# Kernel optimization log

Measured on AMD Instinct MI355X. Metric: run time of the kernel, lower is better.

## Reference

```python
import jax, jax.numpy as jnp
import numpy as np

N, H, V = 4096, 1024, 16384


def setup_inputs() -> dict:
    key = jax.random.key(0)
    k1, k2, k3, k4 = jax.random.split(key, 4)
    _input = jax.random.normal(k1, (N, H), dtype=jnp.float32)
    weight = jax.random.normal(k2, (V, H), dtype=jnp.float32) * (1.0 / np.sqrt(H))
    target = jax.random.normal(k3, (N, V), dtype=jnp.float32)
    bias = jax.random.normal(k4, (V,), dtype=jnp.float32)
    return {"_input": _input, "weight": weight, "target": target, "bias": bias}


def reference(_input, weight, target, bias):
    # Fused linear + MSE with reduction='mean':
    # logits = _input @ weight.T + bias  -> (N, V)
    # loss = mean((logits - target)**2) over all N*V elements
    logits = jnp.einsum("nh,vh->nv", _input, weight) + bias
    diff = logits - target
    return jnp.mean(diff * diff)
```

## Files before the change

### kernel.cpp

```cpp
#include <hip/hip_runtime.h>
#include <hip/hip_bf16.h>
#include <stdint.h>

#define N_ 4096
#define H_ 1024
#define V_ 16384

using bf16x8 = __attribute__((ext_vector_type(8))) short;
using f32x4  = __attribute__((ext_vector_type(4))) float;

__device__ inline ushort f2bf(float f) {
    union { float f; uint32_t u; } v; v.f = f;
    uint32_t u = v.u;
    uint32_t lsb = (u >> 16) & 1u;
    u += 0x7fffu + lsb;
    return (ushort)(u >> 16);
}

__global__ void cast_f32_to_bf16(const float* __restrict__ in, ushort* __restrict__ out) {
    size_t i = ((size_t)blockIdx.x * blockDim.x + threadIdx.x) * 8;
    float4 a = *(const float4*)(in + i);
    float4 b = *(const float4*)(in + i + 4);
    union { ushort h[8]; uint4 u; } p;
    p.h[0] = f2bf(a.x); p.h[1] = f2bf(a.y); p.h[2] = f2bf(a.z); p.h[3] = f2bf(a.w);
    p.h[4] = f2bf(b.x); p.h[5] = f2bf(b.y); p.h[6] = f2bf(b.z); p.h[7] = f2bf(b.w);
    *(uint4*)(out + i) = p.u;
}

#define BM 128
#define BN 128
#define BK 32

__global__ __launch_bounds__(256, 2) void gemm_mse(
    const ushort* __restrict__ Abf,
    const ushort* __restrict__ Wbf,
    const float*  __restrict__ target,
    const float*  __restrict__ bias,
    float* __restrict__ partials)
{
    __shared__ ushort As[BM * BK];
    __shared__ ushort Bs[BN * BK];
    __shared__ float red[4];

    const int tid  = threadIdx.x;
    const int w    = tid >> 6;
    const int lane = tid & 63;
    const int quad = lane >> 4;
    const int l16  = lane & 15;
    const int wm   = w >> 1;
    const int wn   = w & 1;

    const int rowBase = blockIdx.y * BM;
    const int colBase = blockIdx.x * BN;

    f32x4 acc[4][4];
#pragma unroll
    for (int i = 0; i < 4; ++i)
#pragma unroll
        for (int j = 0; j < 4; ++j) acc[i][j] = (f32x4){0.f, 0.f, 0.f, 0.f};

    const int ldrow = lane >> 2;
    const int ldk   = (lane & 3) * 8;

    for (int k0 = 0; k0 < H_; k0 += BK) {
        __syncthreads();
#pragma unroll
        for (int c = 0; c < 2; ++c) {
            const int chunk = w * 2 + c;
            const ushort* ga = Abf + (size_t)(rowBase + chunk * 16 + ldrow) * H_ + k0 + ldk;
            __builtin_amdgcn_global_load_lds(
                (const __attribute__((address_space(1))) void*)ga,
                (__attribute__((address_space(3))) void*)(As + chunk * 512), 16, 0, 0);
            const ushort* gb = Wbf + (size_t)(colBase + chunk * 16 + ldrow) * H_ + k0 + ldk;
            __builtin_amdgcn_global_load_lds(
                (const __attribute__((address_space(1))) void*)gb,
                (__attribute__((address_space(3))) void*)(Bs + chunk * 512), 16, 0, 0);
        }
        __syncthreads();

        bf16x8 af[4], bfr[4];
#pragma unroll
        for (int i = 0; i < 4; ++i)
            af[i] = *(const bf16x8*)(As + (wm * 64 + i * 16 + l16) * BK + quad * 8);
#pragma unroll
        for (int j = 0; j < 4; ++j)
            bfr[j] = *(const bf16x8*)(Bs + (wn * 64 + j * 16 + l16) * BK + quad * 8);
#pragma unroll
        for (int i = 0; i < 4; ++i)
#pragma unroll
            for (int j = 0; j < 4; ++j)
                acc[i][j] = __builtin_amdgcn_mfma_f32_16x16x32_bf16(af[i], bfr[j], acc[i][j], 0, 0, 0);
    }

    float sum = 0.f;
    float biasj[4];
#pragma unroll
    for (int j = 0; j < 4; ++j) biasj[j] = bias[colBase + wn * 64 + j * 16 + l16];

#pragma unroll
    for (int i = 0; i < 4; ++i) {
#pragma unroll
        for (int r = 0; r < 4; ++r) {
            const int gm = rowBase + wm * 64 + i * 16 + quad * 4 + r;
            const float* trow = target + (size_t)gm * V_ + colBase + wn * 64 + l16;
#pragma unroll
            for (int j = 0; j < 4; ++j) {
                float d = acc[i][j][r] + biasj[j] - trow[j * 16];
                sum += d * d;
            }
        }
    }

#pragma unroll
    for (int off = 32; off; off >>= 1) sum += __shfl_down(sum, off, 64);
    if (lane == 0) red[w] = sum;
    __syncthreads();
    if (tid == 0)
        partials[blockIdx.y * gridDim.x + blockIdx.x] = red[0] + red[1] + red[2] + red[3];
}

__global__ void finalize_kernel(const float* __restrict__ partials, float* __restrict__ out, int n) {
    float s = 0.f;
    for (int i = threadIdx.x; i < n; i += 256) s += partials[i];
#pragma unroll
    for (int off = 32; off; off >>= 1) s += __shfl_down(s, off, 64);
    __shared__ float red[4];
    const int w = threadIdx.x >> 6, lane = threadIdx.x & 63;
    if (lane == 0) red[w] = s;
    __syncthreads();
    if (threadIdx.x == 0)
        out[0] = (red[0] + red[1] + red[2] + red[3]) * (1.0f / ((float)N_ * (float)V_));
}

extern "C" void kernel_launch(void* const* d_in, const int* in_sizes, int n_in,
                              void* d_out, int out_size, void* d_ws, size_t ws_size,
                              hipStream_t stream) {
    const float* input  = (const float*)d_in[0];
    const float* weight = (const float*)d_in[1];
    const float* target = (const float*)d_in[2];
    const float* bias   = (const float*)d_in[3];
    float* out = (float*)d_out;

    ushort* Abf = (ushort*)d_ws;
    ushort* Wbf = Abf + (size_t)N_ * H_;
    float* partials = (float*)(Wbf + (size_t)V_ * H_);

    cast_f32_to_bf16<<<(N_ * H_) / (256 * 8), 256, 0, stream>>>(input, Abf);
    cast_f32_to_bf16<<<(V_ * H_) / (256 * 8), 256, 0, stream>>>(weight, Wbf);

    dim3 grid(V_ / BN, N_ / BM);
    gemm_mse<<<grid, 256, 0, stream>>>(Abf, Wbf, target, bias, partials);

    finalize_kernel<<<1, 256, 0, stream>>>(partials, out, (V_ / BN) * (N_ / BM));
}
```

Baseline: 529.2 us.

## Switch GEMM to 32x32x16 bf16 MFMA with fragment-ordered LDS layout

Replaces the 4x4 grid of 16x16x32 MFMAs per wave with a 2x2 grid of 32x32x16 MFMAs, taking two k-steps per BK tile. The global-to-LDS loads are rearranged so each 512-element LDS chunk holds exactly one wave's operand fragment, letting each lane read its operand with a single contiguous 16-byte load. The epilogue is remapped to the 32x32 accumulator row layout. The intent is fewer MFMA issues and simpler LDS reads; the larger instruction has different latency and accumulator register pressure.

New measurement: 634.0 us. 1.2x slower.

```diff
diff --git a/kernel.cpp b/kernel.cpp
--- a/kernel.cpp
+++ b/kernel.cpp
@@ -7,7 +7,7 @@
 #define V_ 16384
 
 using bf16x8 = __attribute__((ext_vector_type(8))) short;
-using f32x4  = __attribute__((ext_vector_type(4))) float;
+using f32x16 = __attribute__((ext_vector_type(16))) float;
 
 __device__ inline ushort f2bf(float f) {
     union { float f; uint32_t u; } v; v.f = f;
@@ -38,74 +38,79 @@
     const float*  __restrict__ bias,
     float* __restrict__ partials)
 {
-    __shared__ ushort As[BM * BK];
-    __shared__ ushort Bs[BN * BK];
+    __shared__ ushort As[8 * 512];
+    __shared__ ushort Bs[8 * 512];
     __shared__ float red[4];
 
     const int tid  = threadIdx.x;
     const int w    = tid >> 6;
     const int lane = tid & 63;
-    const int quad = lane >> 4;
-    const int l16  = lane & 15;
+    const int l32  = lane & 31;
+    const int half = lane >> 5;
     const int wm   = w >> 1;
     const int wn   = w & 1;
 
     const int rowBase = blockIdx.y * BM;
     const int colBase = blockIdx.x * BN;
 
-    f32x4 acc[4][4];
+    f32x16 acc[2][2];
 #pragma unroll
-    for (int i = 0; i < 4; ++i)
+    for (int i = 0; i < 2; ++i)
 #pragma unroll
-        for (int j = 0; j < 4; ++j) acc[i][j] = (f32x4){0.f, 0.f, 0.f, 0.f};
-
-    const int ldrow = lane >> 2;
-    const int ldk   = (lane & 3) * 8;
+        for (int j = 0; j < 2; ++j)
+#pragma unroll
+            for (int r = 0; r < 16; ++r) acc[i][j][r] = 0.f;
 
     for (int k0 = 0; k0 < H_; k0 += BK) {
         __syncthreads();
 #pragma unroll
         for (int c = 0; c < 2; ++c) {
-            const int chunk = w * 2 + c;
-            const ushort* ga = Abf + (size_t)(rowBase + chunk * 16 + ldrow) * H_ + k0 + ldk;
+            const int chunkid = w * 2 + c;
+            const int rb = chunkid >> 1;
+            const int kh = chunkid & 1;
+            const ushort* ga = Abf + (size_t)(rowBase + rb * 32 + l32) * H_ + k0 + kh * 16 + half * 8;
             __builtin_amdgcn_global_load_lds(
                 (const __attribute__((address_space(1))) void*)ga,
-                (__attribute__((address_space(3))) void*)(As + chunk * 512), 16, 0, 0);
-            const ushort* gb = Wbf + (size_t)(colBase + chunk * 16 + ldrow) * H_ + k0 + ldk;
+                (__attribute__((address_space(3))) void*)(As + chunkid * 512), 16, 0, 0);
+            const ushort* gb = Wbf + (size_t)(colBase + rb * 32 + l32) * H_ + k0 + kh * 16 + half * 8;
             __builtin_amdgcn_global_load_lds(
                 (const __attribute__((address_space(1))) void*)gb,
-                (__attribute__((address_space(3))) void*)(Bs + chunk * 512), 16, 0, 0);
+                (__attribute__((address_space(3))) void*)(Bs + chunkid * 512), 16, 0, 0);
         }
         __syncthreads();
 
-        bf16x8 af[4], bfr[4];
 #pragma unroll
-        for (int i = 0; i < 4; ++i)
-            af[i] = *(const bf16x8*)(As + (wm * 64 + i * 16 + l16) * BK + quad * 8);
+        for (int s = 0; s < 2; ++s) {
+            bf16x8 af[2], bq[2];
 #pragma unroll
-        for (int j = 0; j < 4; ++j)
-            bfr[j] = *(const bf16x8*)(Bs + (wn * 64 + j * 16 + l16) * BK + quad * 8);
+            for (int i = 0; i < 2; ++i)
+                af[i] = *(const bf16x8*)(As + (((wm * 2 + i) << 1) + s) * 512 + lane * 8);
 #pragma unroll
-        for (int i = 0; i < 4; ++i)
+            for (int j = 0; j < 2; ++j)
+                bq[j] = *(const bf16x8*)(Bs + (((wn * 2 + j) << 1) + s) * 512 + lane * 8);
 #pragma unroll
-            for (int j = 0; j < 4; ++j)
-                acc[i][j] = __builtin_amdgcn_mfma_f32_16x16x32_bf16(af[i], bfr[j], acc[i][j], 0, 0, 0);
+            for (int i = 0; i < 2; ++i)
+#pragma unroll
+                for (int j = 0; j < 2; ++j)
+                    acc[i][j] = __builtin_amdgcn_mfma_f32_32x32x16_bf16(af[i], bq[j], acc[i][j], 0, 0, 0);
+        }
     }
 
     float sum = 0.f;
-    float biasj[4];
+    float biasj[2];
 #pragma unroll
-    for (int j = 0; j < 4; ++j) biasj[j] = bias[colBase + wn * 64 + j * 16 + l16];
+    for (int j = 0; j < 2; ++j) biasj[j] = bias[colBase + wn * 64 + j * 32 + l32];
 
 #pragma unroll
-    for (int i = 0; i < 4; ++i) {
+    for (int i = 0; i < 2; ++i) {
 #pragma unroll
-        for (int r = 0; r < 4; ++r) {
-            const int gm = rowBase + wm * 64 + i * 16 + quad * 4 + r;
-            const float* trow = target + (size_t)gm * V_ + colBase + wn * 64 + l16;
+        for (int r = 0; r < 16; ++r) {
+            const int row = (r & 3) + 8 * (r >> 2) + 4 * half;
+            const int gm = rowBase + wm * 64 + i * 32 + row;
+            const float* trow = target + (size_t)gm * V_ + colBase + wn * 64 + l32;
 #pragma unroll
-            for (int j = 0; j < 4; ++j) {
-                float d = acc[i][j][r] + biasj[j] - trow[j * 16];
+            for (int j = 0; j < 2; ++j) {
+                float d = acc[i][j][r] + biasj[j] - trow[j * 32];
                 sum += d * d;
             }
         }
```
